# Performance work log

Measured on AMD Instinct MI355X. Metric: run time of the kernel, lower is better.

## Reference

```python
import jax, jax.numpy as jnp
import numpy as np

TOP_K = 2


def setup_inputs() -> dict:
    key = jax.random.key(0)
    k0, k1, k2, k3 = jax.random.split(key, 4)
    N, D, O, E = 131072, 512, 512, 16
    H = D // 4  # gate hidden: gate_input_size // 4
    x = jax.random.normal(k0, (N, D), dtype=jnp.float32)
    # gate MLP params (task_bh=0 gate; Linear weights stored as [in, out])
    Wg1 = jax.random.normal(k1, (D, H), dtype=jnp.float32) / np.sqrt(D).astype(np.float32)
    bg1 = jnp.zeros((H,), jnp.float32)
    Wg2 = jax.random.normal(k2, (H, E), dtype=jnp.float32) * 0.02
    bg2 = jnp.zeros((E,), jnp.float32)
    # per-expert Linear(D, O) weights stacked [E, D, O]
    We = jax.random.normal(k3, (E, D, O), dtype=jnp.float32) / np.sqrt(D).astype(np.float32)
    be = jnp.zeros((E, O), jnp.float32)
    return {"x": x, "Wg1": Wg1, "bg1": bg1, "Wg2": Wg2, "bg2": bg2,
            "We": We, "be": be, "task_bh": 0}


def reference(x, Wg1, bg1, Wg2, bg2, We, be, task_bh):
    # --- top_k_gating (noisy_gating=False path) ---
    h = jax.nn.gelu(x @ Wg1 + bg1, approximate=False)  # nn.GELU default is exact erf
    logits = h @ Wg2 + bg2                              # [N, E]
    probs = jax.nn.softmax(logits, axis=1) + 1e-4       # [N, E]
    top_g, top_i = jax.lax.top_k(probs, TOP_K)          # [N, K]
    N, E = probs.shape
    # dense gate matrix: zeros.scatter(1, top_k_indices, top_k_gates)
    gates = jnp.zeros_like(probs).at[jnp.arange(N)[:, None], top_i].set(top_g)
    # --- dispatch / per-expert GEMM / combine ---
    # Equivalent to: gather tokens per expert, expert Linear, scale by gate,
    # scatter-add back. Since gates[n, e] == 0 for unselected experts, the
    # combined output equals sum_e gates[:, e] * (x @ We[e] + be[e]).
    def body(acc, ewb):
        W_e, b_e, g_e = ewb                      # [D,O], [O], [N]
        return acc + g_e[:, None] * (x @ W_e + b_e), None
    init = jnp.zeros((N, We.shape[2]), x.dtype)
    out, _ = jax.lax.scan(body, init, (We, be, gates.T))
    return out
```

## Files before the change

### kernel.cpp

```cpp
#include <hip/hip_runtime.h>
#include <cstdint>
#include <math.h>


#define NTOK 131072
#define DDIM 512
#define NT 16

typedef _Float16 f16;
typedef f16   f16x8 __attribute__((ext_vector_type(8)));
typedef float f32x4 __attribute__((ext_vector_type(4)));

__device__ __forceinline__ void load_lds16(const void* g, void* l){
  __builtin_amdgcn_global_load_lds(
      (const __attribute__((address_space(1))) void*)(uintptr_t)g,
      (__attribute__((address_space(3))) void*)(uintptr_t)l, 16, 0, 0);
}

__device__ __forceinline__ f32x4 MFMAH(f16x8 a, f16x8 b, f32x4 c){
  return __builtin_amdgcn_mfma_f32_16x16x32_f16(a, b, c, 0, 0, 0);
}

__device__ __forceinline__ f16x8 readF64h(const char* buf, int r, int q){
  return *(const f16x8*)(buf + r*128 + ((q ^ (r & 7)) << 4));
}
__device__ __forceinline__ f16x8 readF32h(const char* buf, int r, int q){
  return *(const f16x8*)(buf + r*64 + ((q ^ (r & 3)) << 4));
}
__device__ __forceinline__ f16x8 pack8f(const float* fv){
  f16x8 v;
  #pragma unroll
  for (int j=0;j<8;++j) v[j] = (f16)fv[j];
  return v;
}

__device__ __forceinline__ void stageB32(const void* grow, char* lds, int tid){
  const char* gb = (const char*)grow;
  #pragma unroll
  for (int i = 0; i < 2; ++i){
    int lin = i*4096 + tid*16;
    int r = lin >> 6;
    int g = (lin >> 4) & 3;
    load_lds16(gb + r*1024 + ((g ^ (r & 3)) << 4), lds + i*4096 + ((tid >> 6) << 10));
  }
}

__global__ void kconv(const float* __restrict__ We, const float* __restrict__ Wg1,
                      const float* __restrict__ Wg2,
                      f16* __restrict__ Wt, f16* __restrict__ W1, char* __restrict__ Wg2f){
  __shared__ float sh[64*65];
  int bx = blockIdx.x, tid = threadIdx.x;
  if (bx < 1024){
    int e = bx >> 6, dt = (bx >> 3) & 7, ot = bx & 7;
    const float* src = We + (size_t)e*262144 + (size_t)dt*64*512 + ot*64;
    #pragma unroll
    for (int it=0; it<16; ++it){ int idx = it*256+tid; int dl = idx>>6, ol = idx&63;
      sh[dl*65+ol] = src[dl*512+ol]; }
    __syncthreads();
    f16* dst = Wt + (size_t)e*262144 + (size_t)ot*64*512 + dt*64;
    #pragma unroll
    for (int it=0; it<16; ++it){ int idx = it*256+tid; int ol = idx>>6, dl = idx&63;
      dst[(size_t)ol*512+dl] = (f16)sh[dl*65+ol]; }
  } else if (bx < 1040){
    int q = bx - 1024;
    int dt = q >> 1, ht = q & 1;
    const float* src = Wg1 + (size_t)dt*64*128 + ht*64;
    #pragma unroll
    for (int it=0; it<16; ++it){ int idx = it*256+tid; int dl = idx>>6, ol = idx&63;
      sh[dl*65+ol] = src[dl*128+ol]; }
    __syncthreads();
    #pragma unroll
    for (int it=0; it<16; ++it){ int idx = it*256+tid; int ol = idx>>6, dl = idx&63;
      W1[(size_t)(ht*64+ol)*512 + dt*64+dl] = (f16)sh[dl*65+ol]; }
  } else {
    int ks = tid >> 6, l = tid & 63;
    int col = l & 15, kb = ks*32 + ((l >> 4) << 3);
    f16x8 v;
    #pragma unroll
    for (int j=0;j<8;++j) v[j] = (f16)Wg2[(kb+j)*16 + col];
    *(f16x8*)(Wg2f + (ks*64+l)*16) = v;
  }
}

__global__ __launch_bounds__(256) void kgate(
    const float* __restrict__ x, const f16* __restrict__ W1, const char* __restrict__ Wg2f,
    const float* __restrict__ bg1, const float* __restrict__ bg2,
    f16* __restrict__ xbf,
    int2* __restrict__ gate_e, float2* __restrict__ gate_g,
    int* __restrict__ refine_cnt, int* __restrict__ refine_list, int* __restrict__ counts)
{
  __shared__ __align__(16) char sm[38912];
  const int BOFF = 8192;
  int tid = threadIdx.x, bid = blockIdx.x;
  int lane = tid & 63, w = tid >> 6, wm = w >> 1, wn = w & 1;
  int l15 = lane & 15, l4 = lane >> 4;
  int t0 = bid * 64;
  int ar = tid >> 2, acq = tid & 3;
  const float* xrow = x + (size_t)(t0 + ar) * DDIM;
  char* xbfb = (char*)xbf;
  f32x4 acc[2][4];
  #pragma unroll
  for (int n=0;n<4;++n){
    float bb = bg1[wn*64 + n*16 + l15];
    f32x4 z = {bb, bb, bb, bb};
    acc[0][n] = z; acc[1][n] = z;
  }
  stageB32(W1, sm + BOFF, tid);
  {
    float fv[8];
    *(float4*)&fv[0] = *(const float4*)(xrow + acq*8);
    *(float4*)&fv[4] = *(const float4*)(xrow + acq*8 + 4);
    f16x8 v8 = pack8f(fv);
    if (xbf) *(f16x8*)(xbfb + (size_t)(t0+ar)*1024 + acq*16) = v8;
    *(f16x8*)(sm + ar*64 + ((acq ^ (ar & 3)) << 4)) = v8;
  }
  for (int ks = 0; ks < 16; ++ks){
    int b = ks & 1;
    asm volatile("s_waitcnt vmcnt(0)" ::: "memory");
    __syncthreads();
    f16x8 v8;
    if (ks < 15){
      int k2 = ks + 1, b2 = k2 & 1;
      stageB32((const char*)W1 + k2*64, sm + BOFF + b2*8192, tid);
      float fv[8];
      *(float4*)&fv[0] = *(const float4*)(xrow + k2*32 + acq*8);
      *(float4*)&fv[4] = *(const float4*)(xrow + k2*32 + acq*8 + 4);
      v8 = pack8f(fv);
      if (xbf) *(f16x8*)(xbfb + (size_t)(t0+ar)*1024 + k2*64 + acq*16) = v8;
    }
    const char* Ab = sm + b*4096;
    const char* Bb = sm + BOFF + b*8192;
    f16x8 ah[2], bh[4];
    #pragma unroll
    for (int m=0;m<2;++m) ah[m] = readF32h(Ab, wm*32 + m*16 + l15, l4);
    #pragma unroll
    for (int n=0;n<4;++n) bh[n] = readF32h(Bb, wn*64 + n*16 + l15, l4);
    #pragma unroll
    for (int m=0;m<2;++m)
      #pragma unroll
      for (int n=0;n<4;++n) acc[m][n] = MFMAH(ah[m], bh[n], acc[m][n]);
    if (ks < 15){
      int b2 = (ks + 1) & 1;
      *(f16x8*)(sm + b2*4096 + ar*64 + ((acq ^ (ar & 3)) << 4)) = v8;
    }
  }
  __syncthreads();
  uint4 wgf[4];
  #pragma unroll
  for (int ksq=0; ksq<4; ++ksq) wgf[ksq] = *(const uint4*)(Wg2f + (ksq*64+lane)*16);
  float* hl = (float*)sm;
  #pragma unroll
  for (int m=0;m<2;++m)
    #pragma unroll
    for (int n=0;n<4;++n)
      #pragma unroll
      for (int j=0;j<4;++j){
        int row = wm*32 + m*16 + (l4 << 2) + j;
        int col = wn*64 + n*16 + l15;
        float uv = acc[m][n][j];
        hl[row*132 + col] = 0.5f * uv * (1.0f + erff(uv * 0.70710678118654752f));
      }
  __syncthreads();
  {
    float bb2 = bg2[l15];
    f32x4 acc2 = {bb2, bb2, bb2, bb2};
    #pragma unroll
    for (int ksq=0; ksq<4; ++ksq){
      const float* hp = (const float*)sm + (w*16 + l15)*132 + ksq*32 + l4*8;
      f16x8 afr;
      #pragma unroll
      for (int j=0;j<8;++j) afr[j] = (f16)hp[j];
      acc2 = MFMAH(afr, *(const f16x8*)&wgf[ksq], acc2);
    }
    float* ll = (float*)(sm + 33792);
    #pragma unroll
    for (int j=0;j<4;++j) ll[(w*16 + l4*4 + j)*16 + l15] = acc2[j];
  }
  int* hist = (int*)(sm + 37888);
  hist[tid] = 0;
  __syncthreads();
  if (tid < 64){
    int t = t0 + tid;
    const float* l = (const float*)(sm + 33792) + tid*16;
    float b1 = -1e30f, b2 = -1e30f, b3 = -1e30f; int e1 = 0, e2 = 0;
    #pragma unroll
    for (int e = 0; e < 16; ++e){
      float v = l[e];
      if (v > b1){ b3 = b2; b2 = b1; e2 = e1; b1 = v; e1 = e; }
      else if (v > b2){ b3 = b2; b2 = v; e2 = e; }
      else if (v > b3){ b3 = v; }
    }
    double s = 0.0;
    #pragma unroll
    for (int e = 0; e < 16; ++e) s += exp((double)l[e] - (double)b1);
    double inv = 1.0 / s;
    gate_e[t] = make_int2(e1, e2);
    gate_g[t] = make_float2((float)(inv + 1e-4), (float)(exp((double)b2 - (double)b1) * inv + 1e-4));
    if (b2 - b3 < 2e-3f){
      int pos = atomicAdd(refine_cnt, 1);
      refine_list[pos] = t;
    }
    int pa = min(e1, e2), pb = max(e1, e2);
    atomicAdd(&hist[pa*16 + pb], 1);
  }
  __syncthreads();
  if (hist[tid]) atomicAdd(&counts[tid], hist[tid]);
}

__global__ __launch_bounds__(128) void krefine(
    const float* __restrict__ x, const float* __restrict__ Wg1, const float* __restrict__ bg1,
    const float* __restrict__ Wg2, const float* __restrict__ bg2,
    const int* __restrict__ refine_cnt, const int* __restrict__ refine_list,
    int2* __restrict__ gate_e, float2* __restrict__ gate_g, int* __restrict__ counts)
{
  __shared__ float  xs[512];
  __shared__ double hd[128];
  __shared__ double ld[16];
  int tid = threadIdx.x;
  int rc = *refine_cnt;
  for (int i = blockIdx.x; i < rc; i += gridDim.x){
    __syncthreads();
    int t = refine_list[i];
    *(float4*)(xs + tid*4) = *(const float4*)(x + (size_t)t*DDIM + tid*4);
    __syncthreads();
    double a = (double)bg1[tid];
    for (int d = 0; d < 512; ++d) a += (double)xs[d] * (double)Wg1[d*128 + tid];
    hd[tid] = 0.5 * a * (1.0 + erf(a * 0.70710678118654752440));
    __syncthreads();
    if (tid < 16){
      double s = (double)bg2[tid];
      for (int k = 0; k < 128; ++k) s += hd[k] * (double)Wg2[k*16 + tid];
      ld[tid] = s;
    }
    __syncthreads();
    if (tid == 0){
      int2 olde = gate_e[t];
      double b1 = -1e300, b2 = -1e300; int e1 = 0, e2 = 0;
      for (int e = 0; e < 16; ++e){
        double v = ld[e];
        if (v > b1){ b2 = b1; e2 = e1; b1 = v; e1 = e; }
        else if (v > b2){ b2 = v; e2 = e; }
      }
      double s = 0.0;
      for (int e = 0; e < 16; ++e) s += exp(ld[e] - b1);
      double inv = 1.0 / s;
      int oldp = min(olde.x, olde.y)*16 + max(olde.x, olde.y);
      int newp = min(e1, e2)*16 + max(e1, e2);
      if (oldp != newp){ atomicSub(&counts[oldp], 1); atomicAdd(&counts[newp], 1); }
      gate_e[t] = make_int2(e1, e2);
      gate_g[t] = make_float2((float)(inv + 1e-4), (float)(exp(b2 - b1) * inv + 1e-4));
    }
  }
}

__global__ void kscan(const int* __restrict__ counts, int* __restrict__ bases,
                      int* __restrict__ tile_pair, int* __restrict__ tile_row0, int* __restrict__ ntiles,
                      int ts){
  int l = threadIdx.x;
  int4 c = *(const int4*)(counts + l*4);
  int s = c.x + c.y + c.z + c.w;
  int ps = s;
  #pragma unroll
  for (int d = 1; d < 64; d <<= 1){ int v = __shfl_up(ps, d); if (l >= d) ps += v; }
  int ex = ps - s;
  bases[4*l+0] = ex;
  bases[4*l+1] = ex + c.x;
  bases[4*l+2] = ex + c.x + c.y;
  bases[4*l+3] = ex + c.x + c.y + c.z;
  if (l == 63) bases[256] = ex + s;
  int t0 = (c.x + ts-1) / ts, t1 = (c.y + ts-1) / ts, t2 = (c.z + ts-1) / ts, t3 = (c.w + ts-1) / ts;
  int tsum = t0 + t1 + t2 + t3;
  int pt = tsum;
  #pragma unroll
  for (int d = 1; d < 64; d <<= 1){ int v = __shfl_up(pt, d); if (l >= d) pt += v; }
  int ext = pt - tsum;
  if (l == 63) *ntiles = ext + tsum;
  int tb = ext;
  int cc[4] = {c.x, c.y, c.z, c.w};
  #pragma unroll
  for (int j = 0; j < 4; ++j){
    int pp = 4*l + j;
    for (int r = 0; r < cc[j]; r += ts){ tile_pair[tb] = pp; tile_row0[tb] = r; ++tb; }
  }
}

__global__ void kscatter(const int2* __restrict__ gate_e, const float2* __restrict__ gate_g,
                         const int* __restrict__ bases, int* __restrict__ cursors,
                         int* __restrict__ pair_tok, float2* __restrict__ pair_g){
  __shared__ int h[256];
  __shared__ int gb[256];
  int tid = threadIdx.x;
  h[tid] = 0; __syncthreads();
  int t = blockIdx.x*256 + tid;
  int2 ee = gate_e[t]; float2 gg = gate_g[t];
  int a, b; float ga, gbv;
  if (ee.x < ee.y){ a = ee.x; b = ee.y; ga = gg.x; gbv = gg.y; }
  else            { a = ee.y; b = ee.x; ga = gg.y; gbv = gg.x; }
  int p = a*16 + b;
  int off = atomicAdd(&h[p], 1);
  __syncthreads();
  if (h[tid]) gb[tid] = bases[tid] + atomicAdd(&cursors[tid], h[tid]);
  __syncthreads();
  int slot = gb[p] + off;
  pair_tok[slot] = t;
  pair_g[slot] = make_float2(ga, gbv);
}

#define SB0 __builtin_amdgcn_sched_barrier(0)
#define PH_MID do{ __builtin_amdgcn_s_barrier(); \
                   asm volatile("s_waitcnt lgkmcnt(0)"); SB0; }while(0)
#define PH_END do{ SB0; __builtin_amdgcn_s_barrier(); }while(0)

#define RDA(hp, mb) do{ \
  _Pragma("unroll") for (int m_=0;m_<4;++m_){ \
    int r_ = ((mb)+m_)*16 + l15; \
    af[m_][0] = readF64h(hp, r_, l4); \
    af[m_][1] = readF64h(hp, r_, 4+l4); }}while(0)
#define RDB(hp, bv, nb) do{ \
  _Pragma("unroll") for (int n_=0;n_<2;++n_){ \
    int r_ = bln + ((nb)+n_)*16 + l15; \
    bv[n_][0] = readF64h(hp, r_, l4); \
    bv[n_][1] = readF64h(hp, r_, 4+l4); }}while(0)
#define MMAC(bv, mb, nb) do{ \
  __builtin_amdgcn_s_setprio(1); \
  _Pragma("unroll") for (int m_=0;m_<4;++m_){ \
    _Pragma("unroll") for (int n_=0;n_<2;++n_){ \
      acc[(mb)+m_][(nb)+n_] = MFMAH(af[m_][0], bv[n_][0], acc[(mb)+m_][(nb)+n_]); \
      acc[(mb)+m_][(nb)+n_] = MFMAH(af[m_][1], bv[n_][1], acc[(mb)+m_][(nb)+n_]); }} \
  __builtin_amdgcn_s_setprio(0); \
}while(0)

__global__ __launch_bounds__(512, 2) void kexpert2(
    const f16* __restrict__ xbf, const f16* __restrict__ Wt, const float* __restrict__ be,
    float* __restrict__ out,
    const int* __restrict__ counts, const int* __restrict__ bases,
    const int* __restrict__ tile_pair, const int* __restrict__ tile_row0, const int* __restrict__ ntiles,
    const int* __restrict__ pair_tok, const float2* __restrict__ pair_g)
{
  __shared__ __align__(16) char sm[134144];
  const int BBASE = 65536, LTOK = 131072, LG = 132096;
  int bid = blockIdx.x;
  int tile = ((bid >> 4) << 3) | (bid & 7);
  int nt = (bid >> 3) & 1;
  if (tile >= *ntiles) return;
  int p = tile_pair[tile], row0 = tile_row0[tile];
  int base = bases[p], cnt = counts[p];
  int eA = p >> 4, eB = p & 15;
  int tid = threadIdx.x, lane = tid & 63, w = tid >> 6;
  int wm = w >> 2, wn = w & 3;
  int l15 = lane & 15, l4 = lane >> 4;
  int bln = (wn & 1) * 64;
  if (tid < 256){
    int rr = row0 + tid; bool v = rr < cnt;
    ((int*)(sm + LTOK))[tid] = v ? pair_tok[base + rr] : -1;
    ((float2*)(sm + LG))[tid] = v ? pair_g[base + rr] : make_float2(0.f, 1.f);
  }
  __syncthreads();

  int rr0 = tid >> 3;
  int sw = ((tid & 7) ^ (rr0 & 7)) << 4;
  const char* xb = (const char*)xbf;
  const char* srcA[2][2];
  #pragma unroll
  for (int h = 0; h < 2; ++h)
    #pragma unroll
    for (int i = 0; i < 2; ++i){
      int tk = ((const int*)(sm + LTOK))[h*128 + i*64 + rr0];
      if (tk < 0) tk = 0;
      srcA[h][i] = xb + (size_t)tk*1024 + sw;
    }
  const char* srcB0 = (const char*)Wt + (size_t)eA*524288 + (size_t)(nt*256 + rr0)*1024 + sw;
  long long edelt = ((long long)eB - eA) * 524288;
  char* dA = sm + w*1024;
  char* dB = sm + BBASE + w*1024;

  auto stA = [&](int t, int h){
    if (t >= NT) return;
    int ks = t & 7, bf_ = t & 1;
    load_lds16(srcA[h][0] + ks*128, dA + bf_*32768 + h*16384);
    load_lds16(srcA[h][1] + ks*128, dA + bf_*32768 + h*16384 + 8192);
  };
  auto stB = [&](int t, int h){
    if (t >= NT) return;
    int ks = t & 7, bf_ = t & 1;
    long long eo = ((t >= 8) ? edelt : 0) + ks*128;
    load_lds16(srcB0 + h*131072 + eo,         dB + bf_*32768 + h*16384);
    load_lds16(srcB0 + h*131072 + 65536 + eo, dB + bf_*32768 + h*16384 + 8192);
  };

  const char* A0 = sm + wm*16384;
  const char* A1 = A0 + 32768;
  const char* B0 = sm + BBASE + (wn >> 1)*16384;
  const char* B1 = B0 + 32768;

  f32x4 acc[8][4];
  #pragma unroll
  for (int m = 0; m < 8; ++m)
    #pragma unroll
    for (int n = 0; n < 4; ++n) acc[m][n] = (f32x4){0.f,0.f,0.f,0.f};

  stA(0,0); stA(0,1); stB(0,0); stB(0,1); stB(1,0); stB(1,1);
  asm volatile("s_waitcnt vmcnt(4)"); SB0;
  __builtin_amdgcn_s_barrier();

  f16x8 af[4][2], bL[2][2], bH[2][2];
  #pragma unroll 1
  for (int i = 0; i < 8; ++i){
    int t0 = 2*i, t1 = t0 + 1;
    RDA(A0, 0); RDB(B0, bL, 0); stA(t1, 0);
    PH_MID; MMAC(bL, 0, 0); PH_END;
    RDB(B0, bH, 2); stA(t1, 1);
    PH_MID; MMAC(bH, 0, 2); PH_END;
    RDA(A0, 4); stB(t0+2, 0);
    PH_MID; MMAC(bH, 4, 2); PH_END;
    stB(t0+2, 1);
    if (i != 7) { asm volatile("s_waitcnt vmcnt(4)"); SB0; }
    else        { asm volatile("s_waitcnt vmcnt(0)"); SB0; }
    PH_MID; MMAC(bL, 4, 0); PH_END;
    RDA(A1, 0); RDB(B1, bL, 0); stA(t0+2, 0);
    PH_MID; MMAC(bL, 0, 0); PH_END;
    RDB(B1, bH, 2); stA(t0+2, 1);
    PH_MID; MMAC(bH, 0, 2); PH_END;
    RDA(A1, 4); stB(t1+2, 0);
    PH_MID; MMAC(bH, 4, 2); PH_END;
    stB(t1+2, 1);
    if (i != 7) { asm volatile("s_waitcnt vmcnt(4)"); SB0; }
    PH_MID; MMAC(bL, 4, 0); PH_END;
    if (i == 3){
      #pragma unroll
      for (int m = 0; m < 8; ++m)
        #pragma unroll
        for (int j = 0; j < 4; ++j){
          int row = wm*128 + m*16 + l4*4 + j;
          float2 g2 = ((const float2*)(sm + LG))[row];
          float r_ = g2.x / g2.y;
          #pragma unroll
          for (int n = 0; n < 4; ++n) acc[m][n][j] *= r_;
        }
    }
  }

  float bcA[4], bcB[4];
  #pragma unroll
  for (int n = 0; n < 4; ++n){
    int col = nt*256 + wn*64 + n*16 + l15;
    bcA[n] = be[(size_t)eA*DDIM + col];
    bcB[n] = be[(size_t)eB*DDIM + col];
  }
  #pragma unroll
  for (int m = 0; m < 8; ++m)
    #pragma unroll
    for (int j = 0; j < 4; ++j){
      int row = wm*128 + m*16 + l4*4 + j;
      int tk = ((const int*)(sm + LTOK))[row];
      if (tk >= 0){
        float2 g2 = ((const float2*)(sm + LG))[row];
        float* orow = out + (size_t)tk*DDIM + nt*256 + wn*64;
        #pragma unroll
        for (int n = 0; n < 4; ++n)
          orow[n*16 + l15] = g2.y*acc[m][n][j] + g2.x*bcA[n] + g2.y*bcB[n];
      }
    }
}

__global__ __launch_bounds__(256, 2) void kexpertF(
    const float* __restrict__ x,
    const f16* __restrict__ Wt, const float* __restrict__ be,
    float* __restrict__ out,
    const int* __restrict__ counts, const int* __restrict__ bases,
    const int* __restrict__ tile_pair, const int* __restrict__ tile_row0, const int* __restrict__ ntiles,
    const int* __restrict__ pair_tok, const float2* __restrict__ pair_g)
{
  __shared__ __align__(16) char sm[67072];
  const int ABUF = 0, BBUF = 32768, LTOK = 65536, LGOFF = 66048;
  int tile = blockIdx.x >> 2, nt = blockIdx.x & 3;
  if (tile >= *ntiles) return;
  int p = tile_pair[tile], row0 = tile_row0[tile];
  int base = bases[p], cnt = counts[p];
  int eA = p >> 4, eB = p & 15;
  int tid = threadIdx.x, lane = tid & 63;
  int w = tid >> 6, wm = w >> 1, wn = w & 1;
  if (tid < 128){
    int rr = row0 + tid; bool v = rr < cnt;
    ((int*)(sm + LTOK))[tid] = v ? pair_tok[base + rr] : -1;
    ((float2*)(sm + LGOFF))[tid] = v ? pair_g[base + rr] : make_float2(0.f, 0.f);
  }
  __syncthreads();
  const char* wb = (const char*)Wt;
  int grp = tid >> 3, gch = tid & 7;
  int swz = (gch ^ (grp & 7)) << 4;
  long long edelt = ((long long)eB - (long long)eA) * 524288;
  const char* srcB[4];
  #pragma unroll
  for (int i = 0; i < 4; ++i)
    srcB[i] = wb + (long long)eA*524288 + (size_t)(nt*128 + i*32 + grp)*1024 + swz;
  int arow = tid >> 1, ach = tid & 1;
  int tkr = ((const int*)(sm + LTOK))[arow];
  if (tkr < 0) tkr = 0;
  const float* xrow = x + (size_t)tkr*DDIM + ach*32;
  int ldst = (w << 10);
  #pragma unroll
  for (int i = 0; i < 4; ++i) load_lds16(srcB[i], sm + BBUF + i*4096 + ldst);
  {
    #pragma unroll
    for (int q2 = 0; q2 < 4; ++q2){
      float fv[8];
      *(float4*)&fv[0] = *(const float4*)(xrow + q2*8);
      *(float4*)&fv[4] = *(const float4*)(xrow + q2*8 + 4);
      f16x8 hv = pack8f(fv);
      int g = ach*4 + q2;
      *(f16x8*)(sm + ABUF + arow*128 + ((g ^ (arow & 7)) << 4)) = hv;
    }
  }
  f32x4 acc[4][4], res[4][4];
  #pragma unroll
  for (int m=0;m<4;++m)
    #pragma unroll
    for (int n=0;n<4;++n) acc[m][n] = (f32x4){0.f,0.f,0.f,0.f};
  for (int u = 0; u < 16; ++u){
    int b = u & 1;
    asm volatile("s_waitcnt vmcnt(0)" ::: "memory");
    __syncthreads();
    int un = u + 1;
    f16x8 hv[4];
    if (un < 16){
      int b2 = un & 1;
      long long aoff = (long long)(un & 7) * 128;
      long long boff = aoff + ((un >> 3) ? edelt : 0);
      #pragma unroll
      for (int i = 0; i < 4; ++i)
        load_lds16(srcB[i] + boff, sm + BBUF + b2*16384 + i*4096 + ldst);
      const float* xr = xrow + (un & 7)*64;
      #pragma unroll
      for (int q2 = 0; q2 < 4; ++q2){
        float fv[8];
        *(float4*)&fv[0] = *(const float4*)(xr + q2*8);
        *(float4*)&fv[4] = *(const float4*)(xr + q2*8 + 4);
        hv[q2] = pack8f(fv);
      }
    }
    const char* Ab = sm + ABUF + b*16384;
    const char* Bb = sm + BBUF + b*16384;
    f16x8 af2[4][2], bf2[4][2];
    #pragma unroll
    for (int m=0;m<4;++m){
      int r = wm*64 + m*16 + (lane & 15);
      af2[m][0] = readF64h(Ab, r, (lane >> 4));
      af2[m][1] = readF64h(Ab, r, 4 + (lane >> 4));
    }
    #pragma unroll
    for (int n=0;n<4;++n){
      int r = wn*64 + n*16 + (lane & 15);
      bf2[n][0] = readF64h(Bb, r, (lane >> 4));
      bf2[n][1] = readF64h(Bb, r, 4 + (lane >> 4));
    }
    #pragma unroll
    for (int m=0;m<4;++m)
      #pragma unroll
      for (int n=0;n<4;++n){
        acc[m][n] = MFMAH(af2[m][0], bf2[n][0], acc[m][n]);
        acc[m][n] = MFMAH(af2[m][1], bf2[n][1], acc[m][n]);
      }
    if (un < 16){
      int b2 = un & 1;
      #pragma unroll
      for (int q2 = 0; q2 < 4; ++q2){
        int g = ach*4 + q2;
        *(f16x8*)(sm + ABUF + b2*16384 + arow*128 + ((g ^ (arow & 7)) << 4)) = hv[q2];
      }
    }
    if (u == 7){
      const float* bev = be + (size_t)eA*DDIM + nt*128;
      float bcol[4];
      #pragma unroll
      for (int n=0;n<4;++n) bcol[n] = bev[wn*64 + n*16 + (lane & 15)];
      #pragma unroll
      for (int m=0;m<4;++m)
        #pragma unroll
        for (int j=0;j<4;++j){
          int row = wm*64 + m*16 + ((lane >> 4) << 2) + j;
          float g = ((const float2*)(sm + LGOFF))[row].x;
          #pragma unroll
          for (int n=0;n<4;++n){
            res[m][n][j] = g * (acc[m][n][j] + bcol[n]);
            acc[m][n][j] = 0.f;
          }
        }
    }
    if (u == 15){
      const float* bev = be + (size_t)eB*DDIM + nt*128;
      float bcol[4];
      #pragma unroll
      for (int n=0;n<4;++n) bcol[n] = bev[wn*64 + n*16 + (lane & 15)];
      #pragma unroll
      for (int m=0;m<4;++m)
        #pragma unroll
        for (int j=0;j<4;++j){
          int row = wm*64 + m*16 + ((lane >> 4) << 2) + j;
          int tk = ((const int*)(sm + LTOK))[row];
          float g = ((const float2*)(sm + LGOFF))[row].y;
          if (tk >= 0){
            float* orow = out + (size_t)tk*DDIM + nt*128;
            #pragma unroll
            for (int n=0;n<4;++n)
              orow[wn*64 + n*16 + (lane & 15)] = res[m][n][j] + g * (acc[m][n][j] + bcol[n]);
          }
        }
    }
  }
}

extern "C" void kernel_launch(void* const* d_in, const int* in_sizes, int n_in,
                              void* d_out, int out_size, void* d_ws, size_t ws_size,
                              hipStream_t stream)
{
  const float* x   = (const float*)d_in[0];
  const float* Wg1 = (const float*)d_in[1];
  const float* bg1 = (const float*)d_in[2];
  const float* Wg2 = (const float*)d_in[3];
  const float* bg2 = (const float*)d_in[4];
  const float* We  = (const float*)d_in[5];
  const float* be  = (const float*)d_in[6];
  float* out = (float*)d_out;
  char* ws = (char*)d_ws;

  f16*  Wt          = (f16*)(ws + 0);
  f16*  W1          = (f16*)(ws + 8388608);
  char* Wg2f        = ws + 8519680;
  char* CTRL        = ws + 8650752;
  int*  refine_cnt  = (int*)(CTRL);
  int*  ntiles      = (int*)(CTRL + 4);
  int*  counts      = (int*)(CTRL + 64);
  int*  cursors     = (int*)(CTRL + 2048);
  int*  bases       = (int*)(CTRL + 4096);
  int2*   gate_e    = (int2*)(ws + 8658944);
  float2* gate_g    = (float2*)(ws + 9707520);
  int*  refine_list = (int*)(ws + 10756096);
  int*  pair_tok    = (int*)(ws + 11280384);
  float2* pair_g    = (float2*)(ws + 11804672);
  int*  tile_pair   = (int*)(ws + 12853248);
  int*  tile_row0   = (int*)(ws + 12863488);
  const size_t XBF_OFF = 16777216ull;
  const size_t XBF_BYTES = (size_t)NTOK * DDIM * 2;
  bool bf16a = ws_size >= XBF_OFF + XBF_BYTES;
  f16* xbf = bf16a ? (f16*)(ws + XBF_OFF) : nullptr;

  hipMemsetAsync(CTRL, 0, 8192, stream);
  hipLaunchKernelGGL(kconv,    dim3(1041), dim3(256), 0, stream, We, Wg1, Wg2, Wt, W1, Wg2f);
  hipLaunchKernelGGL(kgate,    dim3(2048), dim3(256), 0, stream, x, W1, Wg2f, bg1, bg2,
                     xbf, gate_e, gate_g, refine_cnt, refine_list, counts);
  hipLaunchKernelGGL(krefine,  dim3(1024), dim3(128), 0, stream, x, Wg1, bg1, Wg2, bg2,
                     refine_cnt, refine_list, gate_e, gate_g, counts);
  hipLaunchKernelGGL(kscan,    dim3(1),    dim3(64),  0, stream, counts, bases, tile_pair, tile_row0, ntiles,
                     bf16a ? 256 : 128);
  hipLaunchKernelGGL(kscatter, dim3(512),  dim3(256), 0, stream, gate_e, gate_g, bases, cursors, pair_tok, pair_g);
  if (bf16a)
    hipLaunchKernelGGL(kexpert2, dim3(1408), dim3(512), 0, stream, xbf, Wt, be, out,
                       counts, bases, tile_pair, tile_row0, ntiles, pair_tok, pair_g);
  else
    hipLaunchKernelGGL(kexpertF, dim3(5120), dim3(256), 0, stream, x, Wt, be, out,
                       counts, bases, tile_pair, tile_row0, ntiles, pair_tok, pair_g);
  (void)in_sizes; (void)n_in; (void)out_size; (void)ws_size;
}
```

Measured before the change: 482.5 us.

## Widen gate K-tile, fp32 softmax, fuse scan into scatter, drop memset

Several changes at once. The gate GEMM now stages 64-wide K tiles, giving 8 iterations instead of 16 and fewer barriers. The gate softmax runs in fp32 instead of double, and the refine threshold is tightened so fewer tokens take the slow refine path. The refine kernel uses split accumulators and launches half as many blocks. The single-block scan kernel is folded into kscatter, with every block recomputing the prefix sum, and the control-buffer memset is replaced by zeroing inside kconv. The goal is to remove launch count and serialized tiny kernels. The risks are near-tie top-k mismatches from the looser fp32 path, and the bases/tile lists written only by block 0 while other blocks use their own local copy.

```diff
diff --git a/kernel.cpp b/kernel.cpp
--- a/kernel.cpp
+++ b/kernel.cpp
@@ -24,9 +24,6 @@
 __device__ __forceinline__ f16x8 readF64h(const char* buf, int r, int q){
   return *(const f16x8*)(buf + r*128 + ((q ^ (r & 7)) << 4));
 }
-__device__ __forceinline__ f16x8 readF32h(const char* buf, int r, int q){
-  return *(const f16x8*)(buf + r*64 + ((q ^ (r & 3)) << 4));
-}
 __device__ __forceinline__ f16x8 pack8f(const float* fv){
   f16x8 v;
   #pragma unroll
@@ -34,20 +31,10 @@
   return v;
 }
 
-__device__ __forceinline__ void stageB32(const void* grow, char* lds, int tid){
-  const char* gb = (const char*)grow;
-  #pragma unroll
-  for (int i = 0; i < 2; ++i){
-    int lin = i*4096 + tid*16;
-    int r = lin >> 6;
-    int g = (lin >> 4) & 3;
-    load_lds16(gb + r*1024 + ((g ^ (r & 3)) << 4), lds + i*4096 + ((tid >> 6) << 10));
-  }
-}
-
 __global__ void kconv(const float* __restrict__ We, const float* __restrict__ Wg1,
                       const float* __restrict__ Wg2,
-                      f16* __restrict__ Wt, f16* __restrict__ W1, char* __restrict__ Wg2f){
+                      f16* __restrict__ Wt, f16* __restrict__ W1, char* __restrict__ Wg2f,
+                      int* __restrict__ ctrl){
   __shared__ float sh[64*65];
   int bx = blockIdx.x, tid = threadIdx.x;
   if (bx < 1024){
@@ -79,6 +66,8 @@
     #pragma unroll
     for (int j=0;j<8;++j) v[j] = (f16)Wg2[(kb+j)*16 + col];
     *(f16x8*)(Wg2f + (ks*64+l)*16) = v;
+    #pragma unroll
+    for (int i = 0; i < 8; ++i) ctrl[tid + i*256] = 0;
   }
 }
 
@@ -89,8 +78,9 @@
     int2* __restrict__ gate_e, float2* __restrict__ gate_g,
     int* __restrict__ refine_cnt, int* __restrict__ refine_list, int* __restrict__ counts)
 {
-  __shared__ __align__(16) char sm[38912];
-  const int BOFF = 8192;
+  __shared__ __align__(16) char sm[49152];
+  const int AOFF = 0;
+  const int BOFF = 16384;
   int tid = threadIdx.x, bid = blockIdx.x;
   int lane = tid & 63, w = tid >> 6, wm = w >> 1, wn = w & 1;
   int l15 = lane & 15, l4 = lane >> 4;
@@ -105,44 +95,52 @@
     f32x4 z = {bb, bb, bb, bb};
     acc[0][n] = z; acc[1][n] = z;
   }
-  stageB32(W1, sm + BOFF, tid);
-  {
-    float fv[8];
-    *(float4*)&fv[0] = *(const float4*)(xrow + acq*8);
-    *(float4*)&fv[4] = *(const float4*)(xrow + acq*8 + 4);
-    f16x8 v8 = pack8f(fv);
-    if (xbf) *(f16x8*)(xbfb + (size_t)(t0+ar)*1024 + acq*16) = v8;
-    *(f16x8*)(sm + ar*64 + ((acq ^ (ar & 3)) << 4)) = v8;
-  }
-  for (int ks = 0; ks < 16; ++ks){
+  auto stageA = [&](int ks, char* abuf){
+    float fv[16];
+    #pragma unroll
+    for (int q=0;q<4;++q) *(float4*)&fv[q*4] = *(const float4*)(xrow + ks*64 + acq*16 + q*4);
+    f16x8 h0 = pack8f(fv), h1 = pack8f(fv+8);
+    *(f16x8*)(abuf + ar*128 + (((acq*2)   ^ (ar & 7)) << 4)) = h0;
+    *(f16x8*)(abuf + ar*128 + (((acq*2+1) ^ (ar & 7)) << 4)) = h1;
+    if (xbf){
+      char* xd = xbfb + (size_t)(t0+ar)*1024 + ks*128 + acq*32;
+      *(f16x8*)xd = h0; *(f16x8*)(xd+16) = h1;
+    }
+  };
+  auto stageB = [&](int ks, char* lds){
+    const char* gb = (const char*)W1 + ks*128;
+    #pragma unroll
+    for (int i = 0; i < 4; ++i){
+      int lin = i*4096 + tid*16;
+      int r = lin >> 7, g = (lin >> 4) & 7;
+      load_lds16(gb + r*1024 + ((g ^ (r & 7)) << 4), lds + i*4096 + ((tid >> 6) << 10));
+    }
+  };
+  stageB(0, sm + BOFF); stageA(0, sm + AOFF);
+  for (int ks = 0; ks < 8; ++ks){
     int b = ks & 1;
     asm volatile("s_waitcnt vmcnt(0)" ::: "memory");
     __syncthreads();
-    f16x8 v8;
-    if (ks < 15){
-      int k2 = ks + 1, b2 = k2 & 1;
-      stageB32((const char*)W1 + k2*64, sm + BOFF + b2*8192, tid);
-      float fv[8];
-      *(float4*)&fv[0] = *(const float4*)(xrow + k2*32 + acq*8);
-      *(float4*)&fv[4] = *(const float4*)(xrow + k2*32 + acq*8 + 4);
-      v8 = pack8f(fv);
-      if (xbf) *(f16x8*)(xbfb + (size_t)(t0+ar)*1024 + k2*64 + acq*16) = v8;
-    }
-    const char* Ab = sm + b*4096;
-    const char* Bb = sm + BOFF + b*8192;
-    f16x8 ah[2], bh[4];
-    #pragma unroll
-    for (int m=0;m<2;++m) ah[m] = readF32h(Ab, wm*32 + m*16 + l15, l4);
-    #pragma unroll
-    for (int n=0;n<4;++n) bh[n] = readF32h(Bb, wn*64 + n*16 + l15, l4);
+    if (ks < 7) stageB(ks+1, sm + BOFF + (b^1)*16384);
+    const char* Ab = sm + AOFF + b*8192;
+    const char* Bb = sm + BOFF + b*16384;
+    f16x8 ah[2][2], bh[4][2];
     #pragma unroll
     for (int m=0;m<2;++m)
       #pragma unroll
-      for (int n=0;n<4;++n) acc[m][n] = MFMAH(ah[m], bh[n], acc[m][n]);
-    if (ks < 15){
-      int b2 = (ks + 1) & 1;
-      *(f16x8*)(sm + b2*4096 + ar*64 + ((acq ^ (ar & 3)) << 4)) = v8;
-    }
+      for (int kf=0;kf<2;++kf) ah[m][kf] = readF64h(Ab, wm*32 + m*16 + l15, kf*4 + l4);
+    #pragma unroll
+    for (int n=0;n<4;++n)
+      #pragma unroll
+      for (int kf=0;kf<2;++kf) bh[n][kf] = readF64h(Bb, wn*64 + n*16 + l15, kf*4 + l4);
+    #pragma unroll
+    for (int m=0;m<2;++m)
+      #pragma unroll
+      for (int n=0;n<4;++n){
+        acc[m][n] = MFMAH(ah[m][0], bh[n][0], acc[m][n]);
+        acc[m][n] = MFMAH(ah[m][1], bh[n][1], acc[m][n]);
+      }
+    if (ks < 7) stageA(ks+1, sm + AOFF + (b^1)*8192);
   }
   __syncthreads();
   uint4 wgf[4];
@@ -172,16 +170,16 @@
       for (int j=0;j<8;++j) afr[j] = (f16)hp[j];
       acc2 = MFMAH(afr, *(const f16x8*)&wgf[ksq], acc2);
     }
-    float* ll = (float*)(sm + 33792);
+    float* ll = (float*)(sm + 36864);
     #pragma unroll
     for (int j=0;j<4;++j) ll[(w*16 + l4*4 + j)*16 + l15] = acc2[j];
   }
-  int* hist = (int*)(sm + 37888);
+  int* hist = (int*)(sm + 40960);
   hist[tid] = 0;
   __syncthreads();
   if (tid < 64){
     int t = t0 + tid;
-    const float* l = (const float*)(sm + 33792) + tid*16;
+    const float* l = (const float*)(sm + 36864) + tid*16;
     float b1 = -1e30f, b2 = -1e30f, b3 = -1e30f; int e1 = 0, e2 = 0;
     #pragma unroll
     for (int e = 0; e < 16; ++e){
@@ -190,13 +188,13 @@
       else if (v > b2){ b3 = b2; b2 = v; e2 = e; }
       else if (v > b3){ b3 = v; }
     }
-    double s = 0.0;
-    #pragma unroll
-    for (int e = 0; e < 16; ++e) s += exp((double)l[e] - (double)b1);
-    double inv = 1.0 / s;
+    float s = 0.f;
+    #pragma unroll
+    for (int e = 0; e < 16; ++e) s += expf(l[e] - b1);
+    float inv = 1.f / s;
     gate_e[t] = make_int2(e1, e2);
-    gate_g[t] = make_float2((float)(inv + 1e-4), (float)(exp((double)b2 - (double)b1) * inv + 1e-4));
-    if (b2 - b3 < 2e-3f){
+    gate_g[t] = make_float2(inv + 1e-4f, expf(b2 - b1) * inv + 1e-4f);
+    if (b2 - b3 < 1e-3f){
       int pos = atomicAdd(refine_cnt, 1);
       refine_list[pos] = t;
     }
@@ -223,14 +221,23 @@
     int t = refine_list[i];
     *(float4*)(xs + tid*4) = *(const float4*)(x + (size_t)t*DDIM + tid*4);
     __syncthreads();
-    double a = (double)bg1[tid];
-    for (int d = 0; d < 512; ++d) a += (double)xs[d] * (double)Wg1[d*128 + tid];
+    double a0=0.0, a1=0.0, a2=0.0, a3=0.0;
+    for (int d = 0; d < 512; d += 4){
+      a0 += (double)xs[d]   * (double)Wg1[(d)*128 + tid];
+      a1 += (double)xs[d+1] * (double)Wg1[(d+1)*128 + tid];
+      a2 += (double)xs[d+2] * (double)Wg1[(d+2)*128 + tid];
+      a3 += (double)xs[d+3] * (double)Wg1[(d+3)*128 + tid];
+    }
+    double a = (double)bg1[tid] + ((a0+a1)+(a2+a3));
     hd[tid] = 0.5 * a * (1.0 + erf(a * 0.70710678118654752440));
     __syncthreads();
     if (tid < 16){
-      double s = (double)bg2[tid];
-      for (int k = 0; k < 128; ++k) s += hd[k] * (double)Wg2[k*16 + tid];
-      ld[tid] = s;
+      double s0=0.0, s1=0.0;
+      for (int k = 0; k < 128; k += 2){
+        s0 += hd[k]   * (double)Wg2[(k)*16 + tid];
+        s1 += hd[k+1] * (double)Wg2[(k+1)*16 + tid];
+      }
+      ld[tid] = (double)bg2[tid] + s0 + s1;
     }
     __syncthreads();
     if (tid == 0){
@@ -253,44 +260,51 @@
   }
 }
 
-__global__ void kscan(const int* __restrict__ counts, int* __restrict__ bases,
-                      int* __restrict__ tile_pair, int* __restrict__ tile_row0, int* __restrict__ ntiles,
-                      int ts){
-  int l = threadIdx.x;
-  int4 c = *(const int4*)(counts + l*4);
-  int s = c.x + c.y + c.z + c.w;
-  int ps = s;
-  #pragma unroll
-  for (int d = 1; d < 64; d <<= 1){ int v = __shfl_up(ps, d); if (l >= d) ps += v; }
-  int ex = ps - s;
-  bases[4*l+0] = ex;
-  bases[4*l+1] = ex + c.x;
-  bases[4*l+2] = ex + c.x + c.y;
-  bases[4*l+3] = ex + c.x + c.y + c.z;
-  if (l == 63) bases[256] = ex + s;
-  int t0 = (c.x + ts-1) / ts, t1 = (c.y + ts-1) / ts, t2 = (c.z + ts-1) / ts, t3 = (c.w + ts-1) / ts;
-  int tsum = t0 + t1 + t2 + t3;
-  int pt = tsum;
-  #pragma unroll
-  for (int d = 1; d < 64; d <<= 1){ int v = __shfl_up(pt, d); if (l >= d) pt += v; }
-  int ext = pt - tsum;
-  if (l == 63) *ntiles = ext + tsum;
-  int tb = ext;
-  int cc[4] = {c.x, c.y, c.z, c.w};
-  #pragma unroll
-  for (int j = 0; j < 4; ++j){
-    int pp = 4*l + j;
-    for (int r = 0; r < cc[j]; r += ts){ tile_pair[tb] = pp; tile_row0[tb] = r; ++tb; }
-  }
-}
-
-__global__ void kscatter(const int2* __restrict__ gate_e, const float2* __restrict__ gate_g,
-                         const int* __restrict__ bases, int* __restrict__ cursors,
-                         int* __restrict__ pair_tok, float2* __restrict__ pair_g){
+__global__ __launch_bounds__(256) void kscatter(
+    const int2* __restrict__ gate_e, const float2* __restrict__ gate_g,
+    const int* __restrict__ counts,
+    int* __restrict__ bases, int* __restrict__ cursors,
+    int* __restrict__ tile_pair, int* __restrict__ tile_row0, int* __restrict__ ntiles,
+    int* __restrict__ pair_tok, float2* __restrict__ pair_g, int ts)
+{
   __shared__ int h[256];
   __shared__ int gb[256];
+  __shared__ int bl[257];
   int tid = threadIdx.x;
-  h[tid] = 0; __syncthreads();
+  h[tid] = 0;
+  if (tid < 64){
+    int l = tid;
+    int4 c = *(const int4*)(counts + l*4);
+    int s = c.x + c.y + c.z + c.w;
+    int ps = s;
+    #pragma unroll
+    for (int d = 1; d < 64; d <<= 1){ int v = __shfl_up(ps, d); if (l >= d) ps += v; }
+    int ex = ps - s;
+    bl[4*l+0] = ex;
+    bl[4*l+1] = ex + c.x;
+    bl[4*l+2] = ex + c.x + c.y;
+    bl[4*l+3] = ex + c.x + c.y + c.z;
+    if (l == 63) bl[256] = ex + s;
+    if (blockIdx.x == 0){
+      *(int4*)(bases + 4*l) = make_int4(bl[4*l], bl[4*l+1], bl[4*l+2], bl[4*l+3]);
+      if (l == 63) bases[256] = ex + s;
+      int t0 = (c.x + ts-1)/ts, t1 = (c.y + ts-1)/ts, t2 = (c.z + ts-1)/ts, t3 = (c.w + ts-1)/ts;
+      int tsum = t0 + t1 + t2 + t3;
+      int pt = tsum;
+      #pragma unroll
+      for (int d = 1; d < 64; d <<= 1){ int v = __shfl_up(pt, d); if (l >= d) pt += v; }
+      int ext = pt - tsum;
+      if (l == 63) *ntiles = ext + tsum;
+      int tb = ext;
+      int cc[4] = {c.x, c.y, c.z, c.w};
+      #pragma unroll
+      for (int j = 0; j < 4; ++j){
+        int pp = 4*l + j;
+        for (int r = 0; r < cc[j]; r += ts){ tile_pair[tb] = pp; tile_row0[tb] = r; ++tb; }
+      }
+    }
+  }
+  __syncthreads();
   int t = blockIdx.x*256 + tid;
   int2 ee = gate_e[t]; float2 gg = gate_g[t];
   int a, b; float ga, gbv;
@@ -299,7 +313,7 @@
   int p = a*16 + b;
   int off = atomicAdd(&h[p], 1);
   __syncthreads();
-  if (h[tid]) gb[tid] = bases[tid] + atomicAdd(&cursors[tid], h[tid]);
+  if (h[tid]) gb[tid] = bl[tid] + atomicAdd(&cursors[tid], h[tid]);
   __syncthreads();
   int slot = gb[p] + off;
   pair_tok[slot] = t;
@@ -645,15 +659,15 @@
   bool bf16a = ws_size >= XBF_OFF + XBF_BYTES;
   f16* xbf = bf16a ? (f16*)(ws + XBF_OFF) : nullptr;
 
-  hipMemsetAsync(CTRL, 0, 8192, stream);
-  hipLaunchKernelGGL(kconv,    dim3(1041), dim3(256), 0, stream, We, Wg1, Wg2, Wt, W1, Wg2f);
+  hipLaunchKernelGGL(kconv,    dim3(1041), dim3(256), 0, stream, We, Wg1, Wg2, Wt, W1, Wg2f,
+                     (int*)CTRL);
   hipLaunchKernelGGL(kgate,    dim3(2048), dim3(256), 0, stream, x, W1, Wg2f, bg1, bg2,
                      xbf, gate_e, gate_g, refine_cnt, refine_list, counts);
-  hipLaunchKernelGGL(krefine,  dim3(1024), dim3(128), 0, stream, x, Wg1, bg1, Wg2, bg2,
+  hipLaunchKernelGGL(krefine,  dim3(512),  dim3(128), 0, stream, x, Wg1, bg1, Wg2, bg2,
                      refine_cnt, refine_list, gate_e, gate_g, counts);
-  hipLaunchKernelGGL(kscan,    dim3(1),    dim3(64),  0, stream, counts, bases, tile_pair, tile_row0, ntiles,
+  hipLaunchKernelGGL(kscatter, dim3(512),  dim3(256), 0, stream, gate_e, gate_g, counts,
+                     bases, cursors, tile_pair, tile_row0, ntiles, pair_tok, pair_g,
                      bf16a ? 256 : 128);
-  hipLaunchKernelGGL(kscatter, dim3(512),  dim3(256), 0, stream, gate_e, gate_g, bases, cursors, pair_tok, pair_g);
   if (bf16a)
     hipLaunchKernelGGL(kexpert2, dim3(1408), dim3(512), 0, stream, xbf, Wt, be, out,
                        counts, bases, tile_pair, tile_row0, ntiles, pair_tok, pair_g);
```

Measured after the change: 461.6 us. 1.05x faster.
